# Performance work log

Measured on AMD Instinct MI355X. Metric: run time of the kernel, lower is better.

## Reference

```python
import jax, jax.numpy as jnp
import numpy as np

X_DIM, Z_DIM, N_HEIGHT = 256, 256, 32
EPS = 1e-5  # BatchNorm1d eps

def _bn(x, g, b):
    # BatchNorm1d in training mode: batch statistics over the point axis
    m = x.mean(0)
    v = x.var(0)
    return (x - m) * jax.lax.rsqrt(v + EPS) * g + b

def setup_inputs() -> dict:
    key = jax.random.key(0)
    ks = jax.random.split(key, 16)
    B, N, F = 2, 120000, 3
    inp = {
        'pt_fea': jax.random.normal(ks[0], (B, N, F), jnp.float32),
        'grid_ind': jax.random.randint(ks[1], (B, N, 2), 0, 256, dtype=jnp.int32).astype(jnp.int64),
        'occupancy': (jax.random.uniform(ks[2], (B, 1, X_DIM, N_HEIGHT, Z_DIM)) < 0.1).astype(jnp.float32),
    }
    dims = [(3, 64), (64, 128), (128, 256), (256, 512)]
    for i, (di, do) in enumerate(dims):
        inp[f'W{i+1}'] = jax.random.normal(ks[3 + i], (di, do), jnp.float32) * 0.02
        inp[f'b{i+1}'] = jnp.zeros((do,), jnp.float32)
    for i, d in enumerate([3, 64, 128, 256]):
        inp[f'g{i}'] = jnp.ones((d,), jnp.float32)
        inp[f'be{i}'] = jnp.zeros((d,), jnp.float32)
    inp['Wc'] = jax.random.normal(ks[10], (512, 32), jnp.float32) * 0.02
    inp['bc'] = jnp.zeros((32,), jnp.float32)
    return inp

def reference(pt_fea, occupancy, W1, b1, W2, b2, W3, b3, W4, b4,
              g0, be0, g1, be1, g2, be2, g3, be3, Wc, bc, grid_ind):
    B, N, F = pt_fea.shape
    feats = pt_fea.reshape(B * N, F)                          # cat over batch
    # PointNet per-point MLP: BN -> (Linear -> BN -> ReLU) x3 -> Linear
    h = _bn(feats, g0, be0)
    h = jax.nn.relu(_bn(h @ W1 + b1, g1, be1))
    h = jax.nn.relu(_bn(h @ W2 + b2, g2, be2))
    h = jax.nn.relu(_bn(h @ W3 + b3, g3, be3))
    h = h @ W4 + b4                                           # [B*N, 512]

    # linear segment id per (batch, x, z) cell; equivalent to unique+scatter_max
    gi = grid_ind.reshape(B * N, 2).astype(jnp.int32)
    batch_idx = jnp.repeat(jnp.arange(B, dtype=jnp.int32), N)
    seg = batch_idx * (X_DIM * Z_DIM) + gi[:, 0] * Z_DIM + gi[:, 1]
    n_cells = B * X_DIM * Z_DIM

    pooled = jax.ops.segment_max(h, seg, num_segments=n_cells)          # [cells, 512]
    cnt = jax.ops.segment_sum(jnp.ones((B * N,), h.dtype), seg, num_segments=n_cells)
    occ_mask = (cnt > 0)[:, None]
    pooled = jnp.where(occ_mask, pooled, 0.0)                           # kill -inf empties

    # feature compression on occupied cells only; empty cells stay exactly 0
    comp = jax.nn.relu(pooled @ Wc + bc)
    comp = jnp.where(occ_mask, comp, 0.0)                               # [cells, 32]

    bev = comp.reshape(B, X_DIM, Z_DIM, -1).transpose(0, 3, 1, 2)       # [B, 32, X, Z]
    # MaxPool2d(k=3, stride=1, pad=1); -inf padding matches torch's implicit -inf pad
    bev = jax.lax.reduce_window(bev, -jnp.inf, jax.lax.max,
                                (1, 1, 3, 3), (1, 1, 1, 1), 'SAME')

    occu = occupancy[:, 0].transpose(0, 2, 1, 3)                        # [B, H, X, Z]
    out = jnp.concatenate([occu, bev], axis=1)                          # [B, H+32, X, Z]
    return out
```

## Files before the change

kernel.cpp:

```cpp
#include <hip/hip_runtime.h>
#include <hip/hip_bf16.h>

#define EPSN 1e-5f

typedef __bf16 bf16x8 __attribute__((ext_vector_type(8)));
typedef float f32x4 __attribute__((ext_vector_type(4)));

__device__ __forceinline__ unsigned encf(float f) {
  unsigned u = __float_as_uint(f);
  return (u & 0x80000000u) ? ~u : (u | 0x80000000u);
}
__device__ __forceinline__ float decf(unsigned u) {
  return (u & 0x80000000u) ? __uint_as_float(u ^ 0x80000000u) : __uint_as_float(~u);
}

__global__ __launch_bounds__(256) void stats_feats(const float* __restrict__ pt, int n,
                                                   float* __restrict__ sums) {
  float a0 = 0, a1 = 0, a2 = 0, q0 = 0, q1 = 0, q2 = 0;
  for (int p = blockIdx.x * 256 + threadIdx.x; p < n; p += gridDim.x * 256) {
    float v0 = pt[3 * p], v1 = pt[3 * p + 1], v2 = pt[3 * p + 2];
    a0 += v0; a1 += v1; a2 += v2;
    q0 += v0 * v0; q1 += v1 * v1; q2 += v2 * v2;
  }
  __shared__ float red[4][6];
  float vals[6] = {a0, a1, a2, q0, q1, q2};
  int lane = threadIdx.x & 63, wv = threadIdx.x >> 6;
#pragma unroll
  for (int k = 0; k < 6; k++) {
    float v = vals[k];
#pragma unroll
    for (int o = 32; o; o >>= 1) v += __shfl_down(v, o, 64);
    if (lane == 0) red[wv][k] = v;
  }
  __syncthreads();
  if (threadIdx.x < 6) {
    float v = red[0][threadIdx.x] + red[1][threadIdx.x] + red[2][threadIdx.x] + red[3][threadIdx.x];
    atomicAdd(&sums[threadIdx.x], v);
  }
}

__global__ void bn_prep(const float* __restrict__ sums, int C, float invN,
                        const float* __restrict__ g, const float* __restrict__ be,
                        float* __restrict__ sc, float* __restrict__ sh) {
  int c = threadIdx.x;
  if (c < C) {
    float m = sums[c] * invN;
    float v = fmaxf(sums[C + c] * invN - m * m, 0.f);
    float s = g[c] * rsqrtf(v + EPSN);
    sc[c] = s;
    sh[c] = be[c] - m * s;
  }
}

__global__ __launch_bounds__(256) void wconv(const float* __restrict__ W,
                                             __hip_bfloat16* __restrict__ Wt, int K, int C) {
  int idx = blockIdx.x * 256 + threadIdx.x;
  if (idx >= K * C) return;
  int k = idx / C, c = idx - k * C;
  Wt[(size_t)c * K + k] = __float2bfloat16(W[idx]);
}

__global__ __launch_bounds__(256) void gemm1_stats(const float* __restrict__ pt,
                                                   const float* __restrict__ W,
                                                   const float* __restrict__ bias,
                                                   const float* __restrict__ scsh,
                                                   __hip_bfloat16* __restrict__ Y,
                                                   int n, float* __restrict__ sums) {
  const int c = threadIdx.x & 63;
  const float w0 = W[c], w1 = W[64 + c], w2 = W[128 + c], bb = bias[c];
  const float s0 = scsh[0], s1 = scsh[1], s2 = scsh[2];
  const float h0 = scsh[4], h1 = scsh[5], h2 = scsh[6];
  float s = 0.f, q = 0.f;
  const int total = n * 64;
  for (int idx = blockIdx.x * 256 + threadIdx.x; idx < total; idx += gridDim.x * 256) {
    int p = idx >> 6;
    float x0 = s0 * pt[3 * p]     + h0;
    float x1 = s1 * pt[3 * p + 1] + h1;
    float x2 = s2 * pt[3 * p + 2] + h2;
    float y = bb + x0 * w0 + x1 * w1 + x2 * w2;
    Y[idx] = __float2bfloat16(y);
    s += y; q += y * y;
  }
  __shared__ float sred[4][64], qred[4][64];
  int wv = threadIdx.x >> 6;
  sred[wv][c] = s; qred[wv][c] = q;
  __syncthreads();
  if (threadIdx.x < 64) {
    float S = sred[0][c] + sred[1][c] + sred[2][c] + sred[3][c];
    float Q = qred[0][c] + qred[1][c] + qred[2][c] + qred[3][c];
    atomicAdd(&sums[c], S);
    atomicAdd(&sums[64 + c], Q);
  }
}

template <int K>
__global__ __launch_bounds__(256) void gemm_mfma(
    const __hip_bfloat16* __restrict__ Yin, const __hip_bfloat16* __restrict__ Wt,
    const float* __restrict__ bias, const float* __restrict__ sc, const float* __restrict__ sh,
    __hip_bfloat16* __restrict__ Yout, int C, float* __restrict__ sums, int nrows,
    const unsigned* __restrict__ perm) {
  constexpr int KS = 64, LDA = 72, LDO = 80;
  __shared__ __align__(16) __hip_bfloat16 hA[128 * LDO];
  __shared__ float sredArr[128], qredArr[128];
  const int t = threadIdx.x;
  const int lane = t & 63, wv = t >> 6;
  const int mh = (wv >> 1) * 64, nh = (wv & 1) * 64;
  const int lm = lane & 15, lq = lane >> 4;
  const int p0 = blockIdx.x * 128;
  const int cb0 = blockIdx.y * 128;

  f32x4 acc[4][4];
#pragma unroll
  for (int i = 0; i < 4; i++)
#pragma unroll
    for (int j = 0; j < 4; j++) acc[i][j] = {0.f, 0.f, 0.f, 0.f};

  for (int k0 = 0; k0 < K; k0 += KS) {
    __syncthreads();
#pragma unroll
    for (int it = 0; it < 4; it++) {
      int idx = it * 256 + t;
      int row = idx >> 3;
      int c8 = (idx & 7) * 8;
      int gp = p0 + row;
      __hip_bfloat16 h8[8];
      if (gp < nrows) {
        uint4 raw = *(const uint4*)(Yin + (size_t)gp * K + k0 + c8);
        const __hip_bfloat16* pr = (const __hip_bfloat16*)&raw;
#pragma unroll
        for (int j = 0; j < 8; j++) {
          float v = sc[k0 + c8 + j] * __bfloat162float(pr[j]) + sh[k0 + c8 + j];
          h8[j] = __float2bfloat16(fmaxf(v, 0.f));
        }
      } else {
#pragma unroll
        for (int j = 0; j < 8; j++) h8[j] = __float2bfloat16(0.f);
      }
      *(uint4*)&hA[row * LDA + c8] = *(const uint4*)h8;
    }
    __syncthreads();
#pragma unroll
    for (int kk = 0; kk < KS; kk += 32) {
      bf16x8 a[4], b[4];
#pragma unroll
      for (int i = 0; i < 4; i++)
        a[i] = *(const bf16x8*)&hA[(mh + i * 16 + lm) * LDA + kk + lq * 8];
#pragma unroll
      for (int j = 0; j < 4; j++)
        b[j] = *(const bf16x8*)(const void*)(Wt + (size_t)(cb0 + nh + j * 16 + lm) * K + k0 + kk + lq * 8);
#pragma unroll
      for (int i = 0; i < 4; i++)
#pragma unroll
        for (int j = 0; j < 4; j++)
          acc[i][j] = __builtin_amdgcn_mfma_f32_16x16x32_bf16(a[i], b[j], acc[i][j], 0, 0, 0);
    }
  }

#pragma unroll
  for (int j = 0; j < 4; j++) {
    float bb = bias[cb0 + nh + j * 16 + lm];
#pragma unroll
    for (int i = 0; i < 4; i++)
#pragma unroll
      for (int r = 0; r < 4; r++) acc[i][j][r] += bb;
  }

  __syncthreads();
  if (t < 128) { sredArr[t] = 0.f; qredArr[t] = 0.f; }
  __syncthreads();

#pragma unroll
  for (int j = 0; j < 4; j++) {
    float s = 0.f, q = 0.f;
#pragma unroll
    for (int i = 0; i < 4; i++)
#pragma unroll
      for (int r = 0; r < 4; r++) {
        int grow = p0 + mh + i * 16 + lq * 4 + r;
        if (grow < nrows) { float v = acc[i][j][r]; s += v; q += v * v; }
      }
    s += __shfl_xor(s, 16); s += __shfl_xor(s, 32);
    q += __shfl_xor(q, 16); q += __shfl_xor(q, 32);
    if (lq == 0) {
      atomicAdd(&sredArr[nh + j * 16 + lm], s);
      atomicAdd(&qredArr[nh + j * 16 + lm], q);
    }
  }

  for (int half = 0; half < 2; half++) {
    __syncthreads();
    if ((wv & 1) == half) {
#pragma unroll
      for (int j = 0; j < 4; j++)
#pragma unroll
        for (int i = 0; i < 4; i++)
#pragma unroll
          for (int r = 0; r < 4; r++)
            hA[(mh + i * 16 + lq * 4 + r) * LDO + j * 16 + lm] = __float2bfloat16(acc[i][j][r]);
    }
    __syncthreads();
    int row = t >> 1, seg = t & 1;
    int gp = p0 + row;
    if (gp < nrows) {
      size_t drow = perm ? (size_t)perm[gp] : (size_t)gp;
      const uint4* src = (const uint4*)&hA[row * LDO + seg * 32];
      uint4* dst = (uint4*)(Yout + drow * C + cb0 + half * 64 + seg * 32);
      dst[0] = src[0]; dst[1] = src[1]; dst[2] = src[2]; dst[3] = src[3];
    }
  }

  if (t < 128) {
    atomicAdd(&sums[cb0 + t], sredArr[t]);
    atomicAdd(&sums[C + cb0 + t], qredArr[t]);
  }
}

__global__ __launch_bounds__(256) void hist_kernel(const int* __restrict__ gi, int perB,
                                                   unsigned* __restrict__ hist) {
  int b = blockIdx.y;
  int p = blockIdx.x * 256 + threadIdx.x;
  if (p < perB) {
    int gp = b * perB + p;
    int c = (gi[2 * gp] & 255) * 256 + (gi[2 * gp + 1] & 255);
    atomicAdd(&hist[b * 65536 + c], 1u);
  }
}
__global__ __launch_bounds__(256) void scan1(const unsigned* __restrict__ hist,
                                             unsigned* __restrict__ cursor,
                                             unsigned* __restrict__ bSums) {
  __shared__ unsigned s[256];
  int b = blockIdx.y;
  int t = threadIdx.x, i = b * 65536 + blockIdx.x * 256 + t;
  unsigned v = hist[i]; s[t] = v; __syncthreads();
  for (int off = 1; off < 256; off <<= 1) {
    unsigned x = (t >= off) ? s[t - off] : 0u; __syncthreads();
    s[t] += x; __syncthreads();
  }
  cursor[i] = s[t] - v;
  if (t == 255) bSums[b * 256 + blockIdx.x] = s[255];
}
__global__ void scan2(unsigned* __restrict__ bSums) {
  __shared__ unsigned s[256];
  int t = threadIdx.x, i = blockIdx.x * 256 + t;
  unsigned v = bSums[i]; s[t] = v; __syncthreads();
  for (int off = 1; off < 256; off <<= 1) {
    unsigned x = (t >= off) ? s[t - off] : 0u; __syncthreads();
    s[t] += x; __syncthreads();
  }
  bSums[i] = s[t] - v;
}
__global__ __launch_bounds__(256) void mk_starts(const unsigned* __restrict__ cursor,
                                                 const unsigned* __restrict__ bSums,
                                                 unsigned* __restrict__ starts, int perB) {
  int b = blockIdx.y;
  int i = blockIdx.x * 256 + threadIdx.x;
  starts[b * 65537 + i] = cursor[b * 65536 + i] + bSums[b * 256 + (i >> 8)];
  if (i == 0) starts[b * 65537 + 65536] = (unsigned)perB;
}
__global__ __launch_bounds__(256) void scatter_kernel(const int* __restrict__ gi, int perB,
                                                      unsigned* __restrict__ cursor,
                                                      const unsigned* __restrict__ bSums,
                                                      unsigned* __restrict__ cells,
                                                      unsigned* __restrict__ invPos) {
  int b = blockIdx.y;
  int p = blockIdx.x * 256 + threadIdx.x;
  if (p < perB) {
    int gp = b * perB + p;
    int c = (gi[2 * gp] & 255) * 256 + (gi[2 * gp + 1] & 255);
    unsigned pos = atomicAdd(&cursor[b * 65536 + c], 1u) + bSums[b * 256 + (c >> 8)];
    if (pos >= (unsigned)perB) pos = (unsigned)perB - 1u;
    cells[b * perB + pos] = (unsigned)c;
    invPos[gp] = (unsigned)(b * perB) + pos;
  }
}

__global__ __launch_bounds__(256, 2) void pool_compress(
    const __hip_bfloat16* __restrict__ Y3, const __hip_bfloat16* __restrict__ Wt4,
    const float* __restrict__ b4, const float* __restrict__ sc, const float* __restrict__ sh,
    const __hip_bfloat16* __restrict__ WcT, const float* __restrict__ bc,
    const unsigned* __restrict__ sortedCell, const unsigned* __restrict__ startsAll,
    float* __restrict__ comp, int perB) {
  constexpr int K = 256, KS = 64, LDA = 72, MLW = 516;
  __shared__ __align__(16) __hip_bfloat16 hA[64 * LDA];
  __shared__ __align__(16) unsigned maxLds[32 * MLW];
  __shared__ unsigned char slotRow[256];
  const int t = threadIdx.x;
  const int lane = t & 63, wv = t >> 6;
  const int lm = lane & 15, lq = lane >> 4;
  const int batch = blockIdx.y;
  const unsigned* starts = startsAll + batch * 65537;
  const int c0 = blockIdx.x * 32;
  const int r0 = (int)starts[c0];
  int n = (int)starts[c0 + 32] - r0;
  if (n > 256) n = 256;
  if (n < 0) n = 0;
  const int nrg = (n + 63) >> 6;
  const size_t rowBase = (size_t)batch * perB + r0;

  for (int i = t; i < n; i += 256)
    slotRow[i] = (unsigned char)((sortedCell[batch * perB + r0 + i] - c0) & 31);
  {
    const uint4 z4 = {0u, 0u, 0u, 0u};
    for (int i = t * 4; i < 32 * MLW; i += 1024) *(uint4*)&maxLds[i] = z4;
  }

  for (int rg = 0; rg < nrg; rg++) {
    const int rbase = rg * 64;
    f32x4 acc[4][8];
#pragma unroll
    for (int i = 0; i < 4; i++)
#pragma unroll
      for (int j = 0; j < 8; j++) acc[i][j] = {0.f, 0.f, 0.f, 0.f};
    for (int k0 = 0; k0 < K; k0 += KS) {
      __syncthreads();
#pragma unroll
      for (int it = 0; it < 2; it++) {
        int idx = it * 256 + t;
        int row = idx >> 3;
        int c8 = (idx & 7) * 8;
        int gr = rbase + row;
        __hip_bfloat16 h8[8];
        if (gr < n) {
          uint4 raw = *(const uint4*)(Y3 + (rowBase + gr) * K + k0 + c8);
          const __hip_bfloat16* pr = (const __hip_bfloat16*)&raw;
#pragma unroll
          for (int j = 0; j < 8; j++) {
            float v = sc[k0 + c8 + j] * __bfloat162float(pr[j]) + sh[k0 + c8 + j];
            h8[j] = __float2bfloat16(fmaxf(v, 0.f));
          }
        } else {
#pragma unroll
          for (int j = 0; j < 8; j++) h8[j] = __float2bfloat16(0.f);
        }
        *(uint4*)&hA[row * LDA + c8] = *(const uint4*)h8;
      }
      __syncthreads();
#pragma unroll
      for (int kk = 0; kk < KS; kk += 32) {
        bf16x8 a[4];
#pragma unroll
        for (int i = 0; i < 4; i++)
          a[i] = *(const bf16x8*)&hA[(i * 16 + lm) * LDA + kk + lq * 8];
#pragma unroll
        for (int j = 0; j < 8; j++) {
          bf16x8 b = *(const bf16x8*)(const void*)(Wt4 + (size_t)(wv * 128 + j * 16 + lm) * K + k0 + kk + lq * 8);
#pragma unroll
          for (int i = 0; i < 4; i++)
            acc[i][j] = __builtin_amdgcn_mfma_f32_16x16x32_bf16(a[i], b, acc[i][j], 0, 0, 0);
        }
      }
    }
#pragma unroll
    for (int i = 0; i < 4; i++) {
      const int base = rbase + i * 16 + lq * 4;
      const int rl = n - base;
      if (rl <= 0) continue;
      const int s0 = slotRow[base];
      const int s1 = (rl > 1) ? (int)slotRow[base + 1] : -1;
      const int s2 = (rl > 2) ? (int)slotRow[base + 2] : -1;
      const int s3 = (rl > 3) ? (int)slotRow[base + 3] : -1;
      const bool m01 = (s1 == s0), m12 = (s2 == s1), m23 = (s3 == s2);
#pragma unroll
      for (int j = 0; j < 8; j++) {
        const int col = wv * 128 + j * 16 + lm;
        float v0 = acc[i][j][0], v1 = acc[i][j][1], v2 = acc[i][j][2], v3 = acc[i][j][3];
        v1 = m01 ? fmaxf(v1, v0) : v1;
        v2 = m12 ? fmaxf(v2, v1) : v2;
        v3 = m23 ? fmaxf(v3, v2) : v3;
        if (!m01)           atomicMax(&maxLds[s0 * MLW + col], encf(v0));
        if (rl > 1 && !m12) atomicMax(&maxLds[s1 * MLW + col], encf(v1));
        if (rl > 2 && !m23) atomicMax(&maxLds[s2 * MLW + col], encf(v2));
        if (rl > 3)         atomicMax(&maxLds[s3 * MLW + col], encf(v3));
      }
    }
  }
  __syncthreads();

  if (wv < 2) {
    f32x4 accC[2];
    accC[0] = {0.f, 0.f, 0.f, 0.f};
    accC[1] = {0.f, 0.f, 0.f, 0.f};
#pragma unroll
    for (int ks = 0; ks < 16; ks++) {
      int koff = ks * 32 + lq * 8;
      const unsigned* mp = &maxLds[(wv * 16 + lm) * MLW + koff];
      uint4 m0 = *(const uint4*)mp;
      uint4 m1 = *(const uint4*)(mp + 4);
      unsigned mu[8] = {m0.x, m0.y, m0.z, m0.w, m1.x, m1.y, m1.z, m1.w};
      __hip_bfloat16 af[8];
#pragma unroll
      for (int j = 0; j < 8; j++)
        af[j] = __float2bfloat16(decf(mu[j]) + b4[koff + j]);
      bf16x8 aa = *(const bf16x8*)af;
#pragma unroll
      for (int jn = 0; jn < 2; jn++) {
        bf16x8 b = *(const bf16x8*)(const void*)(WcT + (size_t)(jn * 16 + lm) * 512 + koff);
        accC[jn] = __builtin_amdgcn_mfma_f32_16x16x32_bf16(aa, b, accC[jn], 0, 0, 0);
      }
    }
#pragma unroll
    for (int jn = 0; jn < 2; jn++) {
      float bb = bc[jn * 16 + lm];
#pragma unroll
      for (int r = 0; r < 4; r++) {
        int cell = c0 + wv * 16 + lq * 4 + r;
        int occ = starts[cell + 1] > starts[cell];
        float v = occ ? fmaxf(accC[jn][r] + bb, 0.f) : 0.f;
        comp[((size_t)batch * 65536 + cell) * 32 + jn * 16 + lm] = v;
      }
    }
  }
}

__global__ __launch_bounds__(256) void maxpool_write(const float* __restrict__ comp,
                                                     float* __restrict__ out) {
  __shared__ float tile[32][65];
  int bid = blockIdx.x;
  int z0 = (bid & 3) * 64, x = (bid >> 2) & 255, b = bid >> 10;
  int f = threadIdx.x & 31, zs = threadIdx.x >> 5;
  for (int zi = 0; zi < 8; zi++) {
    int z = z0 + zi * 8 + zs;
    float m = -3.402823466e38f;
    for (int dx = -1; dx <= 1; dx++) {
      int xx = x + dx;
      if (xx < 0 || xx > 255) continue;
      for (int dz = -1; dz <= 1; dz++) {
        int zz = z + dz;
        if (zz < 0 || zz > 255) continue;
        m = fmaxf(m, comp[(size_t)((b << 16) + (xx << 8) + zz) * 32 + f]);
      }
    }
    tile[f][zi * 8 + zs] = m;
  }
  __syncthreads();
  int f2 = threadIdx.x >> 3, seg = threadIdx.x & 7;
  float* dst = out + ((size_t)(b * 64 + 32 + f2) * 256 + x) * 256 + z0 + seg * 8;
#pragma unroll
  for (int u = 0; u < 8; u++) dst[u] = tile[f2][seg * 8 + u];
}

__global__ __launch_bounds__(256) void occu_write(const float* __restrict__ occ,
                                                  float* __restrict__ out) {
  int idx = blockIdx.x * 256 + threadIdx.x;
  int z = idx & 255, x = (idx >> 8) & 255, hh = (idx >> 16) & 31, b = idx >> 21;
  out[((size_t)(b * 64 + hh) * 256 + x) * 256 + z] =
      occ[((size_t)((b * 256 + x) * 32 + hh)) * 256 + z];
}

extern "C" void kernel_launch(void* const* d_in, const int* in_sizes, int n_in,
                              void* d_out, int out_size, void* d_ws, size_t ws_size,
                              hipStream_t stream) {
  const float* pt_fea   = (const float*)d_in[0];
  const int*   grid_ind = (const int*)d_in[1];
  const float* occup    = (const float*)d_in[2];
  const float* W1 = (const float*)d_in[3];  const float* b1 = (const float*)d_in[4];
  const float* W2 = (const float*)d_in[5];  const float* b2 = (const float*)d_in[6];
  const float* W3 = (const float*)d_in[7];  const float* b3 = (const float*)d_in[8];
  const float* W4 = (const float*)d_in[9];  const float* b4 = (const float*)d_in[10];
  const float* g0 = (const float*)d_in[11]; const float* be0 = (const float*)d_in[12];
  const float* g1 = (const float*)d_in[13]; const float* be1 = (const float*)d_in[14];
  const float* g2 = (const float*)d_in[15]; const float* be2 = (const float*)d_in[16];
  const float* g3 = (const float*)d_in[17]; const float* be3 = (const float*)d_in[18];
  const float* Wc = (const float*)d_in[19]; const float* bc = (const float*)d_in[20];
  float* out = (float*)d_out;

  const int nPts = in_sizes[0] / 3;
  const int perB = nPts / 2;
  const float invN = 1.f / (float)nPts;

  char* ws = (char*)d_ws;
  float* stats = (float*)ws;
  float* scsh  = (float*)(ws + 4096);
  float* sums0 = stats;        float* sums1 = stats + 16;
  float* sums2 = stats + 160;  float* sums3 = stats + 416;
  float* sc0 = scsh;
  float* sc1 = scsh + 16;   float* sh1 = scsh + 80;
  float* sc2 = scsh + 144;  float* sh2 = scsh + 272;
  float* sc3 = scsh + 400;  float* sh3 = scsh + 656;
  __hip_bfloat16* Wt2 = (__hip_bfloat16*)(ws + 8192);
  __hip_bfloat16* Wt3 = (__hip_bfloat16*)(ws + 24576);
  __hip_bfloat16* Wt4 = (__hip_bfloat16*)(ws + 90112);
  __hip_bfloat16* WcT = (__hip_bfloat16*)(ws + 352256);
  char* S0 = ws + 385024;
  __hip_bfloat16* Y1 = (__hip_bfloat16*)S0;
  __hip_bfloat16* Y2 = (__hip_bfloat16*)(S0 + 30720000ll);
  __hip_bfloat16* Y3 = (__hip_bfloat16*)(S0 + 92160000ll);
  float* comp       = (float*)S0;
  char* sortBase    = S0 + 17000000ll;
  unsigned* hist    = (unsigned*)sortBase;
  unsigned* cursor  = hist + 2 * 65536;
  unsigned* bSums   = cursor + 2 * 65536;
  unsigned* startsA = bSums + 1024;
  unsigned* cells   = startsA + 131080;
  unsigned* invPos  = cells + 2 * perB;

  hipMemsetAsync(stats, 0, 4096, stream);

  wconv<<<(64 * 128 + 255) / 256, 256, 0, stream>>>(W2, Wt2, 64, 128);
  wconv<<<(128 * 256 + 255) / 256, 256, 0, stream>>>(W3, Wt3, 128, 256);
  wconv<<<(256 * 512 + 255) / 256, 256, 0, stream>>>(W4, Wt4, 256, 512);
  wconv<<<(512 * 32 + 255) / 256, 256, 0, stream>>>(Wc, WcT, 512, 32);

  stats_feats<<<256, 256, 0, stream>>>(pt_fea, nPts, sums0);
  bn_prep<<<1, 256, 0, stream>>>(sums0, 3, invN, g0, be0, sc0, scsh + 4);

  gemm1_stats<<<512, 256, 0, stream>>>(pt_fea, W1, b1, scsh, Y1, nPts, sums1);
  bn_prep<<<1, 256, 0, stream>>>(sums1, 64, invN, g1, be1, sc1, sh1);

  gemm_mfma<64><<<dim3(nPts / 128, 1), 256, 0, stream>>>(Y1, Wt2, b2, sc1, sh1, Y2, 128, sums2, nPts, nullptr);
  bn_prep<<<1, 256, 0, stream>>>(sums2, 128, invN, g2, be2, sc2, sh2);

  hipMemsetAsync(hist, 0, 2 * 65536 * 4, stream);
  const int pgrid = (perB + 255) / 256;
  hist_kernel<<<dim3(pgrid, 2), 256, 0, stream>>>(grid_ind, perB, hist);
  scan1<<<dim3(256, 2), 256, 0, stream>>>(hist, cursor, bSums);
  scan2<<<2, 256, 0, stream>>>(bSums);
  mk_starts<<<dim3(256, 2), 256, 0, stream>>>(cursor, bSums, startsA, perB);
  scatter_kernel<<<dim3(pgrid, 2), 256, 0, stream>>>(grid_ind, perB, cursor, bSums, cells, invPos);

  gemm_mfma<128><<<dim3(nPts / 128, 2), 256, 0, stream>>>(Y2, Wt3, b3, sc2, sh2, Y3, 256, sums3, nPts, invPos);
  bn_prep<<<1, 256, 0, stream>>>(sums3, 256, invN, g3, be3, sc3, sh3);

  pool_compress<<<dim3(2048, 2), 256, 0, stream>>>(
      Y3, Wt4, b4, sc3, sh3, WcT, bc, cells, startsA, comp, perB);

  maxpool_write<<<2048, 256, 0, stream>>>(comp, out);
  occu_write<<<16384, 256, 0, stream>>>(occup, out);
}
```

Measured before the change: 708.1 us.

## Trim pool_compress MFMA tiles to live rows, merge weight-convert and epilogue kernels

Pool_compress now picks 1, 2 or 4 sixteen-row MFMA subtiles per 64-row group based on how many rows remain, so partially filled row groups skip both the padded loads and the MFMA work. The four weight-conversion launches become one kernel, and the maxpool and occupancy-copy kernels merge into one epilogue launch whose occupancy copy now moves float4 per thread instead of scalars. Together these target wasted MFMA work on sparse cells, per-launch overhead and narrow memory accesses, at the cost of three template instantiations of the row-group body (more code, possibly different register use).

```diff
diff --git a/kernel.cpp b/kernel.cpp
--- a/kernel.cpp
+++ b/kernel.cpp
@@ -5,6 +5,8 @@
 
 typedef __bf16 bf16x8 __attribute__((ext_vector_type(8)));
 typedef float f32x4 __attribute__((ext_vector_type(4)));
+
+template <int V> struct ICst { static constexpr int value = V; };
 
 __device__ __forceinline__ unsigned encf(float f) {
   unsigned u = __float_as_uint(f);
@@ -52,12 +54,20 @@
   }
 }
 
-__global__ __launch_bounds__(256) void wconv(const float* __restrict__ W,
-                                             __hip_bfloat16* __restrict__ Wt, int K, int C) {
+__global__ __launch_bounds__(256) void wconv4(
+    const float* __restrict__ W2, const float* __restrict__ W3,
+    const float* __restrict__ W4, const float* __restrict__ Wc,
+    __hip_bfloat16* __restrict__ Wt2, __hip_bfloat16* __restrict__ Wt3,
+    __hip_bfloat16* __restrict__ Wt4, __hip_bfloat16* __restrict__ WcT) {
   int idx = blockIdx.x * 256 + threadIdx.x;
-  if (idx >= K * C) return;
-  int k = idx / C, c = idx - k * C;
-  Wt[(size_t)c * K + k] = __float2bfloat16(W[idx]);
+  const float* W; __hip_bfloat16* Wt; int K, C, l;
+  if (idx < 8192)        { W = W2; Wt = Wt2; K = 64;  C = 128; l = idx; }
+  else if (idx < 40960)  { W = W3; Wt = Wt3; K = 128; C = 256; l = idx - 8192; }
+  else if (idx < 172032) { W = W4; Wt = Wt4; K = 256; C = 512; l = idx - 40960; }
+  else if (idx < 188416) { W = Wc; Wt = WcT; K = 512; C = 32;  l = idx - 172032; }
+  else return;
+  int k = l / C, c = l - k * C;
+  Wt[(size_t)c * K + k] = __float2bfloat16(W[l]);
 }
 
 __global__ __launch_bounds__(256) void gemm1_stats(const float* __restrict__ pt,
@@ -304,18 +314,16 @@
     for (int i = t * 4; i < 32 * MLW; i += 1024) *(uint4*)&maxLds[i] = z4;
   }
 
-  for (int rg = 0; rg < nrg; rg++) {
-    const int rbase = rg * 64;
-    f32x4 acc[4][8];
-#pragma unroll
-    for (int i = 0; i < 4; i++)
+  auto rgBody = [&](int rbase, auto SC) {
+    constexpr int S = decltype(SC)::value;
+    f32x4 acc[S][8];
+#pragma unroll
+    for (int i = 0; i < S; i++)
 #pragma unroll
       for (int j = 0; j < 8; j++) acc[i][j] = {0.f, 0.f, 0.f, 0.f};
     for (int k0 = 0; k0 < K; k0 += KS) {
       __syncthreads();
-#pragma unroll
-      for (int it = 0; it < 2; it++) {
-        int idx = it * 256 + t;
+      for (int idx = t; idx < S * 128; idx += 256) {
         int row = idx >> 3;
         int c8 = (idx & 7) * 8;
         int gr = rbase + row;
@@ -337,21 +345,21 @@
       __syncthreads();
 #pragma unroll
       for (int kk = 0; kk < KS; kk += 32) {
-        bf16x8 a[4];
-#pragma unroll
-        for (int i = 0; i < 4; i++)
+        bf16x8 a[S];
+#pragma unroll
+        for (int i = 0; i < S; i++)
           a[i] = *(const bf16x8*)&hA[(i * 16 + lm) * LDA + kk + lq * 8];
 #pragma unroll
         for (int j = 0; j < 8; j++) {
           bf16x8 b = *(const bf16x8*)(const void*)(Wt4 + (size_t)(wv * 128 + j * 16 + lm) * K + k0 + kk + lq * 8);
 #pragma unroll
-          for (int i = 0; i < 4; i++)
+          for (int i = 0; i < S; i++)
             acc[i][j] = __builtin_amdgcn_mfma_f32_16x16x32_bf16(a[i], b, acc[i][j], 0, 0, 0);
         }
       }
     }
 #pragma unroll
-    for (int i = 0; i < 4; i++) {
+    for (int i = 0; i < S; i++) {
       const int base = rbase + i * 16 + lq * 4;
       const int rl = n - base;
       if (rl <= 0) continue;
@@ -373,6 +381,14 @@
         if (rl > 3)         atomicMax(&maxLds[s3 * MLW + col], encf(v3));
       }
     }
+  };
+
+  for (int rg = 0; rg < nrg; rg++) {
+    const int rbase = rg * 64;
+    const int nlive = n - rbase;
+    if (nlive > 32)      rgBody(rbase, ICst<4>{});
+    else if (nlive > 16) rgBody(rbase, ICst<2>{});
+    else                 rgBody(rbase, ICst<1>{});
   }
   __syncthreads();
 
@@ -412,39 +428,39 @@
   }
 }
 
-__global__ __launch_bounds__(256) void maxpool_write(const float* __restrict__ comp,
-                                                     float* __restrict__ out) {
-  __shared__ float tile[32][65];
+__global__ __launch_bounds__(256) void epilogue_write(const float* __restrict__ comp,
+                                                      const float* __restrict__ occ,
+                                                      float* __restrict__ out) {
   int bid = blockIdx.x;
-  int z0 = (bid & 3) * 64, x = (bid >> 2) & 255, b = bid >> 10;
-  int f = threadIdx.x & 31, zs = threadIdx.x >> 5;
-  for (int zi = 0; zi < 8; zi++) {
-    int z = z0 + zi * 8 + zs;
-    float m = -3.402823466e38f;
-    for (int dx = -1; dx <= 1; dx++) {
-      int xx = x + dx;
-      if (xx < 0 || xx > 255) continue;
-      for (int dz = -1; dz <= 1; dz++) {
-        int zz = z + dz;
-        if (zz < 0 || zz > 255) continue;
-        m = fmaxf(m, comp[(size_t)((b << 16) + (xx << 8) + zz) * 32 + f]);
-      }
-    }
-    tile[f][zi * 8 + zs] = m;
-  }
-  __syncthreads();
-  int f2 = threadIdx.x >> 3, seg = threadIdx.x & 7;
-  float* dst = out + ((size_t)(b * 64 + 32 + f2) * 256 + x) * 256 + z0 + seg * 8;
-#pragma unroll
-  for (int u = 0; u < 8; u++) dst[u] = tile[f2][seg * 8 + u];
-}
-
-__global__ __launch_bounds__(256) void occu_write(const float* __restrict__ occ,
-                                                  float* __restrict__ out) {
-  int idx = blockIdx.x * 256 + threadIdx.x;
-  int z = idx & 255, x = (idx >> 8) & 255, hh = (idx >> 16) & 31, b = idx >> 21;
-  out[((size_t)(b * 64 + hh) * 256 + x) * 256 + z] =
-      occ[((size_t)((b * 256 + x) * 32 + hh)) * 256 + z];
+  if (bid < 2048) {
+    __shared__ float tile[32][65];
+    int z0 = (bid & 3) * 64, x = (bid >> 2) & 255, b = bid >> 10;
+    int f = threadIdx.x & 31, zs = threadIdx.x >> 5;
+    for (int zi = 0; zi < 8; zi++) {
+      int z = z0 + zi * 8 + zs;
+      float m = -3.402823466e38f;
+      for (int dx = -1; dx <= 1; dx++) {
+        int xx = x + dx;
+        if (xx < 0 || xx > 255) continue;
+        for (int dz = -1; dz <= 1; dz++) {
+          int zz = z + dz;
+          if (zz < 0 || zz > 255) continue;
+          m = fmaxf(m, comp[(size_t)((b << 16) + (xx << 8) + zz) * 32 + f]);
+        }
+      }
+      tile[f][zi * 8 + zs] = m;
+    }
+    __syncthreads();
+    int f2 = threadIdx.x >> 3, seg = threadIdx.x & 7;
+    float* dst = out + ((size_t)(b * 64 + 32 + f2) * 256 + x) * 256 + z0 + seg * 8;
+#pragma unroll
+    for (int u = 0; u < 8; u++) dst[u] = tile[f2][seg * 8 + u];
+  } else {
+    int oidx = (bid - 2048) * 256 + threadIdx.x;
+    int z4 = oidx & 63, x = (oidx >> 6) & 255, hh = (oidx >> 14) & 31, b = oidx >> 19;
+    const float4 v = *(const float4*)(occ + ((((size_t)b * 256 + x) * 32 + hh) * 256 + z4 * 4));
+    *(float4*)(out + (((size_t)(b * 64 + hh) * 256 + x) * 256 + z4 * 4)) = v;
+  }
 }
 
 extern "C" void kernel_launch(void* const* d_in, const int* in_sizes, int n_in,
@@ -496,10 +512,7 @@
 
   hipMemsetAsync(stats, 0, 4096, stream);
 
-  wconv<<<(64 * 128 + 255) / 256, 256, 0, stream>>>(W2, Wt2, 64, 128);
-  wconv<<<(128 * 256 + 255) / 256, 256, 0, stream>>>(W3, Wt3, 128, 256);
-  wconv<<<(256 * 512 + 255) / 256, 256, 0, stream>>>(W4, Wt4, 256, 512);
-  wconv<<<(512 * 32 + 255) / 256, 256, 0, stream>>>(Wc, WcT, 512, 32);
+  wconv4<<<736, 256, 0, stream>>>(W2, W3, W4, Wc, Wt2, Wt3, Wt4, WcT);
 
   stats_feats<<<256, 256, 0, stream>>>(pt_fea, nPts, sums0);
   bn_prep<<<1, 256, 0, stream>>>(sums0, 3, invN, g0, be0, sc0, scsh + 4);
@@ -524,6 +537,5 @@
   pool_compress<<<dim3(2048, 2), 256, 0, stream>>>(
       Y3, Wt4, b4, sc3, sh3, WcT, bc, cells, startsA, comp, perB);
 
-  maxpool_write<<<2048, 256, 0, stream>>>(comp, out);
-  occu_write<<<16384, 256, 0, stream>>>(occup, out);
-}
+  epilogue_write<<<6144, 256, 0, stream>>>(comp, occup, out);
+}
```

Result: slower. 900.4 us (+27.1%).
